# Optimization experiments

Hardware: AMD Instinct MI355X
Metric: run time of the kernel (lower is better)

The kernel has to match this reference:

```python
import jax, jax.numpy as jnp
import numpy as np

B = 256      # batch
D = 31       # per-mode feature dim (before bias-1 column)
FUSED = (D + 1) ** 3  # 32768
H1, H2, NCLS = 1024, 256, 4


def setup_inputs() -> dict:
    key = jax.random.key(0)
    ks = jax.random.split(key, 9)
    s = lambda fan_in: 1.0 / np.sqrt(fan_in)
    return {
        "x0": jax.random.normal(ks[0], (B, D), dtype=jnp.float32),
        "x1": jax.random.normal(ks[1], (B, D), dtype=jnp.float32),
        "x2": jax.random.normal(ks[2], (B, D), dtype=jnp.float32),
        "W1": jax.random.uniform(ks[3], (FUSED, H1), jnp.float32, -s(FUSED), s(FUSED)),
        "b1": jax.random.uniform(ks[4], (H1,), jnp.float32, -s(FUSED), s(FUSED)),
        "W2": jax.random.uniform(ks[5], (H1, H2), jnp.float32, -s(H1), s(H1)),
        "b2": jax.random.uniform(ks[6], (H2,), jnp.float32, -s(H1), s(H1)),
        "W3": jax.random.uniform(ks[7], (H2, NCLS), jnp.float32, -s(H2), s(H2)),
        "b3": jax.random.uniform(ks[8], (NCLS,), jnp.float32, -s(H2), s(H2)),
    }


def reference(x0, x1, x2, W1, b1, W2, b2, W3, b3):
    ones = jnp.ones((x0.shape[0], 1), dtype=x0.dtype)
    z0 = jnp.concatenate([x0, ones], axis=1)  # [B, D+1]
    z1 = jnp.concatenate([x1, ones], axis=1)
    z2 = jnp.concatenate([x2, ones], axis=1)
    # Batched triple outer product (vectorized over B, replacing the per-sample loop)
    fused = jnp.einsum("bi,bj,bk->bijk", z0, z1, z2).reshape(x0.shape[0], -1)  # [B, (D+1)^3]
    h = jax.nn.relu(fused @ W1 + b1)
    h = jax.nn.relu(h @ W2 + b2)
    return h @ W3 + b3  # [B, NCLS]
```

## Files before the change

kernel.cpp:

```cpp
#include <hip/hip_runtime.h>


typedef _Float16 half8 __attribute__((ext_vector_type(8)));
typedef _Float16 half4 __attribute__((ext_vector_type(4)));
typedef float f32x4 __attribute__((ext_vector_type(4)));

#define KSPLIT 32

__global__ __launch_bounds__(512, 2) void k1_gemm(
    const float* __restrict__ x0, const float* __restrict__ x1,
    const float* __restrict__ x2, const float* __restrict__ W1,
    _Float16* __restrict__ partial)
{
    __shared__ _Float16 z1L[256 * 36];
    __shared__ _Float16 x2L[256 * 32];

    const int tid  = threadIdx.x;
    const int nt   = blockIdx.x & 7;
    const int ks   = blockIdx.x >> 3;
    const int lane = tid & 63;
    const int w    = __builtin_amdgcn_readfirstlane(tid >> 6);
    const int nl   = lane & 15;
    const int g    = lane >> 4;

    for (int idx = tid; idx < 256 * 32; idx += 512) {
        int b = idx >> 5, j = idx & 31;
        z1L[b * 36 + j] = (_Float16)((j < 31) ? x1[b * 31 + j] : 1.0f);
        x2L[b * 32 + j] = (_Float16)((j < 31) ? x2[b * 31 + j] : 1.0f);
    }
    __syncthreads();

    half8 z2v[16];
#pragma unroll
    for (int ms = 0; ms < 16; ++ms) {
        int b = ms * 16 + nl;
        float v0 = (ks < 31) ? x0[b * 31 + ks] : 1.0f;
        half8 xv = *(const half8*)&x2L[b * 32 + g * 8];
        z2v[ms] = xv * (_Float16)v0;
    }

    const float* gw = W1 + ((size_t)ks << 20) + nt * 128 + w * 16;
    const int vbase = g * 8192 + nl;

    float rx[4][8];
#pragma unroll
    for (int s = 0; s < 4; ++s)
#pragma unroll
        for (int e = 0; e < 8; ++e)
            rx[s][e] = gw[s * 32768 + vbase + e * 1024];

    f32x4 acc[16] = {};
    half4 z1q[16];

#pragma unroll
    for (int grp = 0; grp < 8; ++grp) {
        const int t0 = grp * 4;
#pragma unroll
        for (int ms = 0; ms < 16; ++ms)
            z1q[ms] = *(const half4*)&z1L[(ms * 16 + nl) * 36 + t0];

#pragma unroll
        for (int TT = 0; TT < 4; ++TT) {
            half8 bh;
#pragma unroll
            for (int e = 0; e < 8; ++e) bh[e] = (_Float16)rx[TT][e];
            if (grp < 7) {
                const int base = (t0 + TT + 4) * 32768 + vbase;
#pragma unroll
                for (int e = 0; e < 8; ++e) rx[TT][e] = gw[base + e * 1024];
            }
#pragma unroll
            for (int ms = 0; ms < 16; ++ms) {
                half8 a = z2v[ms] * z1q[ms][TT];
                acc[ms] = __builtin_amdgcn_mfma_f32_16x16x32_f16(a, bh, acc[ms], 0, 0, 0);
            }
        }
    }

    _Float16* pout = partial + ((size_t)ks << 18) + nt * 128 + w * 16 + nl;
#pragma unroll
    for (int ms = 0; ms < 16; ++ms)
#pragma unroll
        for (int r = 0; r < 4; ++r)
            pout[(ms * 16 + g * 4 + r) * 1024] = (_Float16)acc[ms][r];
}

__global__ __launch_bounds__(256) void k2_reduce(
    const _Float16* __restrict__ partial, const float* __restrict__ b1,
    float* __restrict__ h1)
{
    int e = blockIdx.x * 256 + threadIdx.x;
    float s = 0.f;
#pragma unroll
    for (int sp = 0; sp < KSPLIT; ++sp) s += (float)partial[((size_t)sp << 18) + e];
    s += b1[e & 1023];
    h1[e] = fmaxf(s, 0.f);
}

__global__ __launch_bounds__(256) void k3_layer2(
    const float* __restrict__ h1, const float* __restrict__ W2,
    float* __restrict__ p2)
{
    __shared__ float h1t[32 * 129];
    __shared__ float w2t[128 * 65];
    const int tid = threadIdx.x;
    const int m0 = blockIdx.x * 32, n0 = blockIdx.y * 64, k0 = blockIdx.z * 128;

    for (int idx = tid; idx < 32 * 128; idx += 256) {
        int m = idx >> 7, kk = idx & 127;
        h1t[m * 129 + kk] = h1[(m0 + m) * 1024 + k0 + kk];
    }
    for (int idx = tid; idx < 128 * 64; idx += 256) {
        int kk = idx >> 6, n = idx & 63;
        w2t[kk * 65 + n] = W2[(k0 + kk) * 256 + n0 + n];
    }
    __syncthreads();

    const int tn = tid & 63, tm = tid >> 6;
    float acc[8] = {};
    for (int kk = 0; kk < 128; ++kk) {
        float wv = w2t[kk * 65 + tn];
#pragma unroll
        for (int r = 0; r < 8; ++r)
            acc[r] += h1t[(tm * 8 + r) * 129 + kk] * wv;
    }
#pragma unroll
    for (int r = 0; r < 8; ++r)
        p2[blockIdx.z * 65536 + (m0 + tm * 8 + r) * 256 + n0 + tn] = acc[r];
}

__global__ __launch_bounds__(256) void k4_final(
    const float* __restrict__ p2, const float* __restrict__ b2,
    const float* __restrict__ W3, const float* __restrict__ b3,
    float* __restrict__ out)
{
    __shared__ float pL[256 * 5];
    const int b = blockIdx.x, n = threadIdx.x;
    float s = 0.f;
#pragma unroll
    for (int sp = 0; sp < 8; ++sp) s += p2[sp * 65536 + b * 256 + n];
    float h2 = fmaxf(s + b2[n], 0.f);
#pragma unroll
    for (int c = 0; c < 4; ++c) pL[n * 5 + c] = h2 * W3[n * 4 + c];
    __syncthreads();

    const int lane = n & 63, w = n >> 6;
    float v = pL[lane * 5 + w] + pL[(lane + 64) * 5 + w] +
              pL[(lane + 128) * 5 + w] + pL[(lane + 192) * 5 + w];
#pragma unroll
    for (int off = 32; off > 0; off >>= 1) v += __shfl_down(v, off);
    if (lane == 0) out[b * 4 + w] = v + b3[w];
}

extern "C" void kernel_launch(void* const* d_in, const int* in_sizes, int n_in,
                              void* d_out, int out_size, void* d_ws, size_t ws_size,
                              hipStream_t stream)
{
    (void)in_sizes; (void)n_in; (void)out_size; (void)ws_size;
    const float* x0 = (const float*)d_in[0];
    const float* x1 = (const float*)d_in[1];
    const float* x2 = (const float*)d_in[2];
    const float* W1 = (const float*)d_in[3];
    const float* b1 = (const float*)d_in[4];
    const float* W2 = (const float*)d_in[5];
    const float* b2 = (const float*)d_in[6];
    const float* W3 = (const float*)d_in[7];
    const float* b3 = (const float*)d_in[8];
    float* out = (float*)d_out;

    _Float16* partial = (_Float16*)d_ws;
    float* h1 = (float*)((char*)d_ws + (size_t)KSPLIT * 262144 * 2);
    float* p2 = h1 + 262144;

    k1_gemm  <<<dim3(256),     dim3(512), 0, stream>>>(x0, x1, x2, W1, partial);
    k2_reduce<<<dim3(1024),    dim3(256), 0, stream>>>(partial, b1, h1);
    k3_layer2<<<dim3(8, 4, 8), dim3(256), 0, stream>>>(h1, W2, p2);
    k4_final <<<dim3(256),     dim3(256), 0, stream>>>(p2, b2, W3, b3, out);
}
```

Measured before the change: 58.05 us.

## Stage W1 tiles through swizzled double-buffered LDS with coalesced loads in layer-1 GEMM

The layer-1 GEMM kernel now uses 1024 threads split into 4 M-groups by 4 N-groups. W1 is loaded with coalesced float2 reads, converted to fp16 and written into a double-buffered, XOR-swizzled LDS tile. Each wave reads its B fragments from that tile, replacing the old strided per-lane global gathers. This adds a barrier per k-step. The reduce kernel is also vectorized to process half2 pairs.

```diff
diff --git a/kernel.cpp b/kernel.cpp
--- a/kernel.cpp
+++ b/kernel.cpp
@@ -3,98 +3,165 @@
 
 typedef _Float16 half8 __attribute__((ext_vector_type(8)));
 typedef _Float16 half4 __attribute__((ext_vector_type(4)));
+typedef _Float16 half2 __attribute__((ext_vector_type(2)));
 typedef float f32x4 __attribute__((ext_vector_type(4)));
+typedef float f32x2 __attribute__((ext_vector_type(2)));
 
 #define KSPLIT 32
 
-__global__ __launch_bounds__(512, 2) void k1_gemm(
+__global__ __launch_bounds__(1024, 4) void k1_gemm(
     const float* __restrict__ x0, const float* __restrict__ x1,
     const float* __restrict__ x2, const float* __restrict__ W1,
     _Float16* __restrict__ partial)
 {
     __shared__ _Float16 z1L[256 * 36];
-    __shared__ _Float16 x2L[256 * 32];
+    __shared__ _Float16 tileF[2 * 128 * 32];
 
     const int tid  = threadIdx.x;
     const int nt   = blockIdx.x & 7;
     const int ks   = blockIdx.x >> 3;
     const int lane = tid & 63;
-    const int w    = __builtin_amdgcn_readfirstlane(tid >> 6);
+    const int w    = tid >> 6;
     const int nl   = lane & 15;
     const int g    = lane >> 4;
-
-    for (int idx = tid; idx < 256 * 32; idx += 512) {
+    const int mh   = w & 3;
+    const int nw   = w >> 2;
+
+    for (int idx = tid; idx < 256 * 32; idx += 1024) {
         int b = idx >> 5, j = idx & 31;
         z1L[b * 36 + j] = (_Float16)((j < 31) ? x1[b * 31 + j] : 1.0f);
-        x2L[b * 32 + j] = (_Float16)((j < 31) ? x2[b * 31 + j] : 1.0f);
+    }
+
+    half8 z2v[4];
+#pragma unroll
+    for (int ms = 0; ms < 4; ++ms) {
+        int b = mh * 64 + ms * 16 + nl;
+        float v0 = (ks < 31) ? x0[b * 31 + ks] : 1.0f;
+#pragma unroll
+        for (int e = 0; e < 8; ++e) {
+            int kp = g * 8 + e;
+            float v2 = (kp < 31) ? x2[b * 31 + kp] : 1.0f;
+            z2v[ms][e] = (_Float16)(v0 * v2);
+        }
+    }
+
+    const int c = lane;
+    const float* gsrc = W1 + ((size_t)ks * 1024 + 2 * w) * 1024 + nt * 128 + 2 * c;
+    const int kpw = w ^ ((c & 7) << 1);
+    const int waddr0 = (2 * c) * 32 + kpw * 2;
+    const int waddr1 = waddr0 + 32;
+
+    int raddr[2][2];
+#pragma unroll
+    for (int ns = 0; ns < 2; ++ns) {
+        int n = nw * 32 + ns * 16 + nl;
+        int sw = ((n >> 1) & 7) << 1;
+#pragma unroll
+        for (int u = 0; u < 2; ++u)
+            raddr[ns][u] = n * 32 + ((g * 4 + 2 * u) ^ sw) * 2;
+    }
+
+    f32x2 rA[2], rB[2];
+    rA[0] = *(const f32x2*)gsrc;
+    rB[0] = *(const f32x2*)(gsrc + 1024);
+    rA[1] = *(const f32x2*)(gsrc + 32768);
+    rB[1] = *(const f32x2*)(gsrc + 32768 + 1024);
+    {
+        half2 w0, w1;
+        w0[0] = (_Float16)rA[0][0]; w0[1] = (_Float16)rB[0][0];
+        w1[0] = (_Float16)rA[0][1]; w1[1] = (_Float16)rB[0][1];
+        *(half2*)&tileF[waddr0] = w0;
+        *(half2*)&tileF[waddr1] = w1;
     }
     __syncthreads();
 
-    half8 z2v[16];
-#pragma unroll
-    for (int ms = 0; ms < 16; ++ms) {
-        int b = ms * 16 + nl;
-        float v0 = (ks < 31) ? x0[b * 31 + ks] : 1.0f;
-        half8 xv = *(const half8*)&x2L[b * 32 + g * 8];
-        z2v[ms] = xv * (_Float16)v0;
-    }
-
-    const float* gw = W1 + ((size_t)ks << 20) + nt * 128 + w * 16;
-    const int vbase = g * 8192 + nl;
-
-    float rx[4][8];
-#pragma unroll
-    for (int s = 0; s < 4; ++s)
-#pragma unroll
-        for (int e = 0; e < 8; ++e)
-            rx[s][e] = gw[s * 32768 + vbase + e * 1024];
-
-    f32x4 acc[16] = {};
-    half4 z1q[16];
-
-#pragma unroll
-    for (int grp = 0; grp < 8; ++grp) {
+    f32x4 acc[4][2] = {};
+    half4 z1q[4];
+
+#define STEP(T_, TT, LOADF, WRITEF)                                            \
+    {                                                                          \
+        if (LOADF) {                                                           \
+            const float* gp = gsrc + (size_t)((T_) + 2) * 32768;               \
+            rA[(TT) & 1] = *(const f32x2*)gp;                                  \
+            rB[(TT) & 1] = *(const f32x2*)(gp + 1024);                         \
+        }                                                                      \
+        if ((TT) == 0) {                                                       \
+            _Pragma("unroll")                                                  \
+            for (int ms = 0; ms < 4; ++ms)                                     \
+                z1q[ms] = *(const half4*)&z1L[(mh * 64 + ms * 16 + nl) * 36 + t0]; \
+        }                                                                      \
+        const _Float16* tb = &tileF[((TT) & 1) * 4096];                        \
+        half4 lo0 = *(const half4*)&tb[raddr[0][0]];                           \
+        half4 hi0 = *(const half4*)&tb[raddr[0][1]];                           \
+        half4 lo1 = *(const half4*)&tb[raddr[1][0]];                           \
+        half4 hi1 = *(const half4*)&tb[raddr[1][1]];                           \
+        half8 bh0 = __builtin_shufflevector(lo0, hi0, 0,1,2,3,4,5,6,7);        \
+        half8 bh1 = __builtin_shufflevector(lo1, hi1, 0,1,2,3,4,5,6,7);        \
+        _Pragma("unroll")                                                      \
+        for (int ms = 0; ms < 4; ++ms) {                                       \
+            half8 a = z2v[ms] * z1q[ms][TT];                                   \
+            acc[ms][0] = __builtin_amdgcn_mfma_f32_16x16x32_f16(a, bh0, acc[ms][0], 0, 0, 0); \
+            acc[ms][1] = __builtin_amdgcn_mfma_f32_16x16x32_f16(a, bh1, acc[ms][1], 0, 0, 0); \
+        }                                                                      \
+        if (WRITEF) {                                                          \
+            half2 w0, w1;                                                      \
+            w0[0] = (_Float16)rA[((TT) + 1) & 1][0];                           \
+            w0[1] = (_Float16)rB[((TT) + 1) & 1][0];                           \
+            w1[0] = (_Float16)rA[((TT) + 1) & 1][1];                           \
+            w1[1] = (_Float16)rB[((TT) + 1) & 1][1];                           \
+            _Float16* tw = &tileF[(((TT) + 1) & 1) * 4096];                    \
+            *(half2*)&tw[waddr0] = w0;                                         \
+            *(half2*)&tw[waddr1] = w1;                                         \
+        }                                                                      \
+        asm volatile("s_waitcnt lgkmcnt(0)\n\ts_barrier" ::: "memory");        \
+    }
+
+    for (int grp = 0; grp < 7; ++grp) {
         const int t0 = grp * 4;
-#pragma unroll
-        for (int ms = 0; ms < 16; ++ms)
-            z1q[ms] = *(const half4*)&z1L[(ms * 16 + nl) * 36 + t0];
-
-#pragma unroll
-        for (int TT = 0; TT < 4; ++TT) {
-            half8 bh;
-#pragma unroll
-            for (int e = 0; e < 8; ++e) bh[e] = (_Float16)rx[TT][e];
-            if (grp < 7) {
-                const int base = (t0 + TT + 4) * 32768 + vbase;
-#pragma unroll
-                for (int e = 0; e < 8; ++e) rx[TT][e] = gw[base + e * 1024];
-            }
-#pragma unroll
-            for (int ms = 0; ms < 16; ++ms) {
-                half8 a = z2v[ms] * z1q[ms][TT];
-                acc[ms] = __builtin_amdgcn_mfma_f32_16x16x32_f16(a, bh, acc[ms], 0, 0, 0);
-            }
+        STEP(t0 + 0, 0, 1, 1)
+        STEP(t0 + 1, 1, 1, 1)
+        STEP(t0 + 2, 2, 1, 1)
+        STEP(t0 + 3, 3, 1, 1)
+    }
+    {
+        const int t0 = 28;
+        STEP(28, 0, 1, 1)
+        STEP(29, 1, 1, 1)
+        STEP(30, 2, 0, 1)
+        STEP(31, 3, 0, 0)
+    }
+#undef STEP
+
+    _Float16* pbase = partial + ((size_t)ks << 18);
+#pragma unroll
+    for (int ms = 0; ms < 4; ++ms)
+#pragma unroll
+        for (int ns = 0; ns < 2; ++ns) {
+            int h = nt * 128 + nw * 32 + ns * 16 + nl;
+            int b0 = mh * 64 + ms * 16 + g * 4;
+#pragma unroll
+            for (int r = 0; r < 4; ++r)
+                pbase[(b0 + r) * 1024 + h] = (_Float16)acc[ms][ns][r];
         }
-    }
-
-    _Float16* pout = partial + ((size_t)ks << 18) + nt * 128 + w * 16 + nl;
-#pragma unroll
-    for (int ms = 0; ms < 16; ++ms)
-#pragma unroll
-        for (int r = 0; r < 4; ++r)
-            pout[(ms * 16 + g * 4 + r) * 1024] = (_Float16)acc[ms][r];
 }
 
 __global__ __launch_bounds__(256) void k2_reduce(
     const _Float16* __restrict__ partial, const float* __restrict__ b1,
     float* __restrict__ h1)
 {
-    int e = blockIdx.x * 256 + threadIdx.x;
-    float s = 0.f;
-#pragma unroll
-    for (int sp = 0; sp < KSPLIT; ++sp) s += (float)partial[((size_t)sp << 18) + e];
-    s += b1[e & 1023];
-    h1[e] = fmaxf(s, 0.f);
+    int e2 = blockIdx.x * 256 + threadIdx.x;
+    const half2* pv = (const half2*)partial;
+    float s0 = 0.f, s1 = 0.f;
+#pragma unroll
+    for (int sp = 0; sp < KSPLIT; ++sp) {
+        half2 v = pv[(size_t)sp * 131072 + e2];
+        s0 += (float)v[0]; s1 += (float)v[1];
+    }
+    int h = (e2 * 2) & 1023;
+    f32x2 o;
+    o[0] = fmaxf(s0 + b1[h], 0.f);
+    o[1] = fmaxf(s1 + b1[h + 1], 0.f);
+    *(f32x2*)&h1[e2 * 2] = o;
 }
 
 __global__ __launch_bounds__(256) void k3_layer2(
@@ -141,7 +208,7 @@
     for (int sp = 0; sp < 8; ++sp) s += p2[sp * 65536 + b * 256 + n];
     float h2 = fmaxf(s + b2[n], 0.f);
 #pragma unroll
-    for (int c = 0; c < 4; ++c) pL[n * 5 + c] = h2 * W3[n * 4 + c];
+    for (int ccls = 0; ccls < 4; ++ccls) pL[n * 5 + ccls] = h2 * W3[n * 4 + ccls];
     __syncthreads();
 
     const int lane = n & 63, w = n >> 6;
@@ -172,8 +239,8 @@
     float* h1 = (float*)((char*)d_ws + (size_t)KSPLIT * 262144 * 2);
     float* p2 = h1 + 262144;
 
-    k1_gemm  <<<dim3(256),     dim3(512), 0, stream>>>(x0, x1, x2, W1, partial);
-    k2_reduce<<<dim3(1024),    dim3(256), 0, stream>>>(partial, b1, h1);
-    k3_layer2<<<dim3(8, 4, 8), dim3(256), 0, stream>>>(h1, W2, p2);
-    k4_final <<<dim3(256),     dim3(256), 0, stream>>>(p2, b2, W3, b3, out);
-}
+    k1_gemm  <<<dim3(256),     dim3(1024), 0, stream>>>(x0, x1, x2, W1, partial);
+    k2_reduce<<<dim3(512),     dim3(256),  0, stream>>>(partial, b1, h1);
+    k3_layer2<<<dim3(8, 4, 8), dim3(256),  0, stream>>>(h1, W2, p2);
+    k4_final <<<dim3(256),     dim3(256),  0, stream>>>(p2, b2, W3, b3, out);
+}
```

New measurement: 53.63 us. -7.6%, faster.
